# Kernel tuning notes

Measured on AMD Instinct MI355X. Metric: run time of the kernel, lower is better.

Reference implementation:

```python
import jax, jax.numpy as jnp
import numpy as np
import math

B, L, HID = 2, 2048, 1024
NH, DH = 16, 64
MASK_VAL = -1000000000.0  # half_precision_flag == False


def setup_inputs() -> dict:
    key = jax.random.key(0)
    ks = jax.random.split(key, 12)
    s = 0.02
    return {
        "queries": jax.random.normal(ks[0], (B, L, HID), jnp.float32),
        "keys": jax.random.normal(ks[1], (B, L, HID), jnp.float32),
        "values": jax.random.normal(ks[2], (B, L, HID), jnp.float32),
        "mask": jax.random.randint(ks[3], (B, L, L), 0, 2, jnp.int32),
        "Wq": jax.random.normal(ks[4], (HID, NH * DH), jnp.float32) * s,
        "bq": jnp.zeros((NH * DH,), jnp.float32),
        "Wk": jax.random.normal(ks[5], (HID, NH * DH), jnp.float32) * s,
        "bk": jnp.zeros((NH * DH,), jnp.float32),
        "Wv": jax.random.normal(ks[6], (HID, NH * DH), jnp.float32) * s,
        "bv": jnp.zeros((NH * DH,), jnp.float32),
        "Wo": jax.random.normal(ks[7], (NH * DH, HID), jnp.float32) * s,
        "bo": jnp.zeros((HID,), jnp.float32),
    }


def reference(queries, keys, values, mask, Wq, bq, Wk, bk, Wv, bv, Wo, bo):
    # Linear projections: (B, L, NH*DH)
    q = queries @ Wq + bq
    k = keys @ Wk + bk
    v = values @ Wv + bv
    # FAITHFUL to original: raw .view(B, NH, -1, DH) without transpose
    q = q.reshape(B, NH, L, DH)
    k = k.reshape(B, NH, L, DH)
    v = v.reshape(B, NH, L, DH)
    # scaled dot-product scores: (B, NH, L, L)
    scores = jnp.einsum("bhqd,bhkd->bhqk", q, k) / math.sqrt(DH)
    scores = jnp.where(mask[:, None, :, :] == 0, MASK_VAL, scores)
    probs = jax.nn.softmax(scores, axis=-1)  # dropout p=0 -> identity
    ctx = jnp.einsum("bhqk,bhkd->bhqd", probs, v)  # (B, NH, L, DH)
    # transpose(1,2) then flatten heads, as in original
    ctx = ctx.transpose(0, 2, 1, 3).reshape(B, L, NH * DH)
    return ctx @ Wo + bo
```

## Files before the change

kernel.cpp:

```cpp
#include <hip/hip_runtime.h>
#include <stdint.h>

typedef __bf16 bf16;
typedef __bf16 bf16x8 __attribute__((ext_vector_type(8)));
typedef __bf16 bf16x4 __attribute__((ext_vector_type(4)));
typedef float  f32x4  __attribute__((ext_vector_type(4)));
typedef short  s16x4  __attribute__((ext_vector_type(4)));
typedef unsigned long long ull;

#define GLOAD16(gptr, lptr)                                                     \
  __builtin_amdgcn_global_load_lds(                                             \
      (const __attribute__((address_space(1))) void*)(gptr),                    \
      (__attribute__((address_space(3))) void*)(lptr), 16, 0, 0)

#define MFMA16(a, b, c) __builtin_amdgcn_mfma_f32_16x16x32_bf16((a), (b), (c), 0, 0, 0)
#define MFMA16K16(a, b, c) __builtin_amdgcn_mfma_f32_16x16x16bf16_1k((a), (b), (c), 0, 0, 0)

static constexpr int B_ = 2, L_ = 2048, NH_ = 16, DH_ = 64;
static constexpr float QSCALE = 0.18033688011112042f;

__global__ void k_cvt3(const float* __restrict__ q, const float* __restrict__ k,
                       const float* __restrict__ v, bf16* __restrict__ outbase) {
  const float* in = blockIdx.y == 0 ? q : (blockIdx.y == 1 ? k : v);
  bf16* out = outbase + (size_t)blockIdx.y * 4194304;
  int i = blockIdx.x * blockDim.x + threadIdx.x;
  const float4 f = ((const float4*)in)[i];
  bf16x4 o = {(bf16)f.x, (bf16)f.y, (bf16)f.z, (bf16)f.w};
  ((bf16x4*)out)[i] = o;
}

__global__ void k_wtrans4(const float* __restrict__ wq, const float* __restrict__ wk,
                          const float* __restrict__ wv, const float* __restrict__ wo,
                          bf16* __restrict__ outbase) {
  const int z = blockIdx.z;
  const float* in = z == 0 ? wq : (z == 1 ? wk : (z == 2 ? wv : wo));
  bf16* out = outbase + (size_t)z * 1048576;
  __shared__ float t[32][33];
  int bx = blockIdx.x * 32, by = blockIdx.y * 32;
  int x = threadIdx.x & 31, y = threadIdx.x >> 5;
#pragma unroll
  for (int r = 0; r < 4; ++r)
    t[y + r * 8][x] = in[(size_t)(by + y + r * 8) * 1024 + bx + x];
  __syncthreads();
#pragma unroll
  for (int r = 0; r < 4; ++r)
    out[(size_t)(bx + y + r * 8) * 1024 + by + x] = (bf16)t[x][y + r * 8];
}

__global__ void k_maskbits(const int* __restrict__ mask, ull* __restrict__ mb) {
  int t = blockIdx.x * blockDim.x + threadIdx.x;
  ull bal = __ballot(mask[t] != 0);
  if ((threadIdx.x & 63) == 0) mb[t >> 6] = bal;
}

__global__ __launch_bounds__(256) void k_gemm3(const bf16* __restrict__ Xb,
                                               const bf16* __restrict__ Wb,
                                               const float* __restrict__ b0,
                                               const float* __restrict__ b1,
                                               const float* __restrict__ b2,
                                               bf16* __restrict__ Ob) {
  const int z = blockIdx.z;
  const bf16* A  = Xb + (size_t)z * 4194304;
  const bf16* Bt = Wb + (size_t)z * 1048576;
  const float* bias = z == 0 ? b0 : (z == 1 ? b1 : b2);
  bf16* C = Ob + (size_t)z * 4194304;
  const int m0 = blockIdx.y * 128, n0 = blockIdx.x * 128;
  __shared__ __align__(16) bf16 As[128 * 64];
  __shared__ __align__(16) bf16 Bs[128 * 64];
  const int tid = threadIdx.x, lane = tid & 63, w = tid >> 6, quad = lane >> 4, l15 = lane & 15;
  const int wm = (w & 1) * 64, wn = (w >> 1) * 64;
  f32x4 acc[4][4] = {};
  for (int kt = 0; kt < 16; ++kt) {
    const int kk = kt * 64;
#pragma unroll
    for (int i = 0; i < 4; ++i) {
      int s = tid + i * 256;
      int r = s >> 3, c = (s & 7) ^ (r & 7);
      GLOAD16(A + (size_t)(m0 + r) * 1024 + kk + c * 8, As + s * 8);
      GLOAD16(Bt + (size_t)(n0 + r) * 1024 + kk + c * 8, Bs + s * 8);
    }
    __syncthreads();
#pragma unroll
    for (int ks = 0; ks < 2; ++ks) {
      bf16x8 af[4], bb[4];
#pragma unroll
      for (int i = 0; i < 4; ++i) {
        int ra = wm + i * 16 + l15, rb = wn + i * 16 + l15;
        af[i] = *(const bf16x8*)(As + (ra * 8 + ((ks * 4 + quad) ^ (ra & 7))) * 8);
        bb[i] = *(const bf16x8*)(Bs + (rb * 8 + ((ks * 4 + quad) ^ (rb & 7))) * 8);
      }
#pragma unroll
      for (int mi = 0; mi < 4; ++mi)
#pragma unroll
        for (int ni = 0; ni < 4; ++ni)
          acc[mi][ni] = MFMA16(af[mi], bb[ni], acc[mi][ni]);
    }
    __syncthreads();
  }
  const float scale = (z == 0) ? QSCALE : 1.0f;
#pragma unroll
  for (int mi = 0; mi < 4; ++mi)
#pragma unroll
    for (int ni = 0; ni < 4; ++ni) {
      int row = m0 + wm + mi * 16 + quad * 4;
      int col = n0 + wn + ni * 16 + l15;
      float bz = bias[col];
      if (z == 2) {
        int b_ = row >> 11, l = row & 2047;
        int hh = l >> 7;
        int i0 = (l & 127) * 16 + (col >> 6);
        int d  = col & 63;
        bf16* dst = C + (size_t)(b_ * 16 + hh) * 131072;
#pragma unroll
        for (int r = 0; r < 4; ++r) {
          int iK = i0 + 16 * r;
          dst[((size_t)(iK >> 2) * 64 + d) * 4 + (iK & 3)] = (bf16)(acc[mi][ni][r] + bz);
        }
      } else {
#pragma unroll
        for (int r = 0; r < 4; ++r)
          C[(size_t)(row + r) * 1024 + col] = (bf16)((acc[mi][ni][r] + bz) * scale);
      }
    }
}

__global__ __launch_bounds__(256) void k_gemmo(const bf16* __restrict__ A,
                                               const bf16* __restrict__ Bt,
                                               const float* __restrict__ bias,
                                               float* __restrict__ C) {
  const int m0 = blockIdx.y * 64, n0 = blockIdx.x * 128;
  __shared__ __align__(16) bf16 As[64 * 32];
  __shared__ __align__(16) bf16 Bs[128 * 32];
  const int tid = threadIdx.x, lane = tid & 63, w = tid >> 6, quad = lane >> 4, l15 = lane & 15;
  const int wn = w * 32;
  f32x4 acc[4][2] = {};
  for (int kt = 0; kt < 32; ++kt) {
    const int kk = kt * 32;
    {
      int r = tid >> 2, c = (tid & 3) ^ ((r >> 1) & 3);
      GLOAD16(A + (size_t)(m0 + r) * 1024 + kk + c * 8, As + tid * 8);
    }
#pragma unroll
    for (int i = 0; i < 2; ++i) {
      int s = tid + i * 256;
      int r = s >> 2, c = (s & 3) ^ ((r >> 1) & 3);
      GLOAD16(Bt + (size_t)(n0 + r) * 1024 + kk + c * 8, Bs + s * 8);
    }
    __syncthreads();
    bf16x8 af[4], bb[2];
#pragma unroll
    for (int i = 0; i < 4; ++i) {
      int ra = i * 16 + l15;
      af[i] = *(const bf16x8*)(As + (ra * 4 + (quad ^ ((ra >> 1) & 3))) * 8);
    }
#pragma unroll
    for (int i = 0; i < 2; ++i) {
      int rb = wn + i * 16 + l15;
      bb[i] = *(const bf16x8*)(Bs + (rb * 4 + (quad ^ ((rb >> 1) & 3))) * 8);
    }
#pragma unroll
    for (int mi = 0; mi < 4; ++mi)
#pragma unroll
      for (int ni = 0; ni < 2; ++ni)
        acc[mi][ni] = MFMA16(af[mi], bb[ni], acc[mi][ni]);
    __syncthreads();
  }
#pragma unroll
  for (int mi = 0; mi < 4; ++mi)
#pragma unroll
    for (int ni = 0; ni < 2; ++ni) {
      int row = m0 + mi * 16 + quad * 4;
      int col = n0 + wn + ni * 16 + l15;
      float bz = bias[col];
#pragma unroll
      for (int r = 0; r < 4; ++r)
        C[(size_t)(row + r) * 1024 + col] = acc[mi][ni][r] + bz;
    }
}

__global__ __launch_bounds__(256) void k_flash(const bf16* __restrict__ Qp,
                                               const bf16* __restrict__ Kp,
                                               const bf16* __restrict__ Vtp,
                                               const ull* __restrict__ mb,
                                               bf16* __restrict__ ctx) {
  const int b = blockIdx.z, h = blockIdx.y, q0 = blockIdx.x * 64;
  const size_t HEAD = 131072;
  const bf16* Q  = Qp  + ((size_t)b * NH_ + h) * HEAD;
  const bf16* K  = Kp  + ((size_t)b * NH_ + h) * HEAD;
  const bf16* Vt = Vtp + ((size_t)b * NH_ + h) * HEAD;
  const ull* mrow = mb + (size_t)b * L_ * 32;

  __shared__ __align__(16) bf16 Ks[2][64 * 64];
  __shared__ __align__(16) bf16 Vs[2][64 * 64];
  __shared__ __align__(16) ull  Ms[2][128];

  const int tid = threadIdx.x, lane = tid & 63, w = tid >> 6, quad = lane >> 4, l15 = lane & 15;

  bf16x8 qf[2];
#pragma unroll
  for (int ks = 0; ks < 2; ++ks)
    qf[ks] = *(const bf16x8*)(Q + (size_t)(q0 + w * 16 + l15) * 64 + ks * 32 + quad * 8);

#pragma unroll
  for (int i = 0; i < 2; ++i) {
    int s = tid + i * 256;
    int key = s >> 3, c = (s & 7) ^ (key & 7);
    GLOAD16(K + (size_t)key * 64 + c * 8, Ks[0] + s * 8);
    GLOAD16(Vt + (size_t)s * 8, Vs[0] + s * 8);
  }
  if (w == 0) GLOAD16(mrow + (size_t)(q0 + lane) * 32, (bf16*)&Ms[0][0] + lane * 8);
  __syncthreads();

  f32x4 accO[4] = {};
  f32x4 accL = {};
  const s16x4 onesf = {0x3F80, 0x3F80, 0x3F80, 0x3F80};

  for (int kt = 0; kt < 32; ++kt) {
    const int cur = kt & 1;
    if (kt + 1 < 32) {
      const int nxt = cur ^ 1;
#pragma unroll
      for (int i = 0; i < 2; ++i) {
        int s = tid + i * 256;
        int key = s >> 3, c = (s & 7) ^ (key & 7);
        GLOAD16(K + (size_t)((kt + 1) * 64 + key) * 64 + c * 8, Ks[nxt] + s * 8);
        GLOAD16(Vt + (size_t)(kt + 1) * 4096 + s * 8, Vs[nxt] + s * 8);
      }
      if ((kt & 1) && w == 0)
        GLOAD16(mrow + (size_t)(q0 + lane) * 32 + (kt + 1),
                (bf16*)&Ms[((kt + 1) >> 1) & 1][0] + lane * 8);
    }

    f32x4 st[4] = {};
#pragma unroll
    for (int ks = 0; ks < 2; ++ks)
#pragma unroll
      for (int kb = 0; kb < 4; ++kb) {
        int key = kb * 16 + l15;
        bf16x8 kf = *(const bf16x8*)(Ks[cur] + (key * 8 + ((ks * 4 + quad) ^ (key & 7))) * 8);
        st[kb] = MFMA16(kf, qf[ks], st[kb]);
      }

    const ull word = Ms[(kt >> 1) & 1][(w * 16 + l15) * 2 + cur];
    s16x4 pf[4];
#pragma unroll
    for (int kb = 0; kb < 4; ++kb) {
      const unsigned nib = (unsigned)(word >> (kb * 16 + quad * 4)) & 0xFu;
      float p0 = (nib & 1u) ? __builtin_amdgcn_exp2f(st[kb][0]) : 0.f;
      float p1 = (nib & 2u) ? __builtin_amdgcn_exp2f(st[kb][1]) : 0.f;
      float p2 = (nib & 4u) ? __builtin_amdgcn_exp2f(st[kb][2]) : 0.f;
      float p3 = (nib & 8u) ? __builtin_amdgcn_exp2f(st[kb][3]) : 0.f;
      bf16x4 pb = {(bf16)p0, (bf16)p1, (bf16)p2, (bf16)p3};
      pf[kb] = __builtin_bit_cast(s16x4, pb);
    }

#pragma unroll
    for (int kb = 0; kb < 4; ++kb)
      accL = MFMA16K16(pf[kb], onesf, accL);

#pragma unroll
    for (int kb = 0; kb < 4; ++kb)
#pragma unroll
      for (int db = 0; db < 4; ++db) {
        s16x4 vf = *(const s16x4*)(Vs[cur] + ((size_t)((kb * 4 + quad) * 64 + db * 16 + l15)) * 4);
        accO[db] = MFMA16K16(pf[kb], vf, accO[db]);
      }
    __syncthreads();
  }

  float rl[4];
#pragma unroll
  for (int r = 0; r < 4; ++r) rl[r] = 1.0f / accL[r];
#pragma unroll
  for (int db = 0; db < 4; ++db) {
    const int col = h * 64 + db * 16 + l15;
#pragma unroll
    for (int r = 0; r < 4; ++r) {
      const int rowg = q0 + w * 16 + quad * 4 + r;
      ctx[((size_t)b * L_ + rowg) * 1024 + col] = (bf16)(accO[db][r] * rl[r]);
    }
  }
}

extern "C" void kernel_launch(void* const* d_in, const int* in_sizes, int n_in,
                              void* d_out, int out_size, void* d_ws, size_t ws_size,
                              hipStream_t stream) {
  (void)in_sizes; (void)n_in; (void)out_size; (void)ws_size;
  const float* q    = (const float*)d_in[0];
  const float* k    = (const float*)d_in[1];
  const float* v    = (const float*)d_in[2];
  const int*   mask = (const int*)d_in[3];
  const float* Wq = (const float*)d_in[4];
  const float* bq = (const float*)d_in[5];
  const float* Wk = (const float*)d_in[6];
  const float* bk = (const float*)d_in[7];
  const float* Wv = (const float*)d_in[8];
  const float* bv = (const float*)d_in[9];
  const float* Wo = (const float*)d_in[10];
  const float* bo = (const float*)d_in[11];
  float* out = (float*)d_out;

  char* ws = (char*)d_ws;
  const size_t SX = (size_t)4096 * 1024 * 2;
  const size_t SW = (size_t)1024 * 1024 * 2;
  bf16* X   = (bf16*)(ws);
  bf16* Wt  = (bf16*)(ws + 3 * SX);
  bf16* QKV = (bf16*)(ws + 3 * SX + 4 * SW);
  bf16* Qp  = QKV;
  bf16* Kp  = QKV + 4194304;
  bf16* Vtp = QKV + 2 * 4194304;
  bf16* Ctx = (bf16*)(ws + 6 * SX + 4 * SW);
  ull* mbits = (ull*)(ws + 7 * SX + 4 * SW);

  dim3 blk(256);
  k_cvt3<<<dim3(4096, 3), blk, 0, stream>>>(q, k, v, X);
  k_wtrans4<<<dim3(32, 32, 4), blk, 0, stream>>>(Wq, Wk, Wv, Wo, Wt);
  k_maskbits<<<32768, blk, 0, stream>>>(mask, mbits);

  k_gemm3<<<dim3(8, 32, 3), blk, 0, stream>>>(X, Wt, bq, bk, bv, QKV);

  k_flash<<<dim3(32, NH_, B_), blk, 0, stream>>>(Qp, Kp, Vtp, mbits, Ctx);

  k_gemmo<<<dim3(8, 64), blk, 0, stream>>>(Ctx, Wt + 3 * 1048576, bo, out);
}
```

Baseline: 291.0 us.

## Merge prep kernels, halve QKV GEMM K-tile, read flash K/V directly from global

```diff
diff --git a/kernel.cpp b/kernel.cpp
--- a/kernel.cpp
+++ b/kernel.cpp
@@ -19,38 +19,47 @@
 static constexpr int B_ = 2, L_ = 2048, NH_ = 16, DH_ = 64;
 static constexpr float QSCALE = 0.18033688011112042f;
 
-__global__ void k_cvt3(const float* __restrict__ q, const float* __restrict__ k,
-                       const float* __restrict__ v, bf16* __restrict__ outbase) {
-  const float* in = blockIdx.y == 0 ? q : (blockIdx.y == 1 ? k : v);
-  bf16* out = outbase + (size_t)blockIdx.y * 4194304;
-  int i = blockIdx.x * blockDim.x + threadIdx.x;
-  const float4 f = ((const float4*)in)[i];
-  bf16x4 o = {(bf16)f.x, (bf16)f.y, (bf16)f.z, (bf16)f.w};
-  ((bf16x4*)out)[i] = o;
-}
-
-__global__ void k_wtrans4(const float* __restrict__ wq, const float* __restrict__ wk,
-                          const float* __restrict__ wv, const float* __restrict__ wo,
-                          bf16* __restrict__ outbase) {
-  const int z = blockIdx.z;
-  const float* in = z == 0 ? wq : (z == 1 ? wk : (z == 2 ? wv : wo));
-  bf16* out = outbase + (size_t)z * 1048576;
+__global__ __launch_bounds__(256) void k_prep(const float* __restrict__ q,
+                                              const float* __restrict__ k,
+                                              const float* __restrict__ v,
+                                              const int* __restrict__ mask,
+                                              const float* __restrict__ wq,
+                                              const float* __restrict__ wk,
+                                              const float* __restrict__ wv,
+                                              const float* __restrict__ wo,
+                                              bf16* __restrict__ X,
+                                              bf16* __restrict__ Wt,
+                                              ull* __restrict__ mb) {
   __shared__ float t[32][33];
-  int bx = blockIdx.x * 32, by = blockIdx.y * 32;
-  int x = threadIdx.x & 31, y = threadIdx.x >> 5;
-#pragma unroll
-  for (int r = 0; r < 4; ++r)
-    t[y + r * 8][x] = in[(size_t)(by + y + r * 8) * 1024 + bx + x];
-  __syncthreads();
-#pragma unroll
-  for (int r = 0; r < 4; ++r)
-    out[(size_t)(bx + y + r * 8) * 1024 + by + x] = (bf16)t[x][y + r * 8];
-}
-
-__global__ void k_maskbits(const int* __restrict__ mask, ull* __restrict__ mb) {
-  int t = blockIdx.x * blockDim.x + threadIdx.x;
-  ull bal = __ballot(mask[t] != 0);
-  if ((threadIdx.x & 63) == 0) mb[t >> 6] = bal;
+  const int bid = blockIdx.x, tid = threadIdx.x;
+  if (bid < 32768) {
+    int tt = bid * 256 + tid;
+    ull bal = __ballot(mask[tt] != 0);
+    if ((tid & 63) == 0) mb[tt >> 6] = bal;
+  } else if (bid < 45056) {
+    int u = bid - 32768;
+    int z = u >> 12, x = u & 4095;
+    const float* in = z == 0 ? q : (z == 1 ? k : v);
+    bf16* out = X + (size_t)z * 4194304;
+    int i = x * 256 + tid;
+    const float4 f = ((const float4*)in)[i];
+    bf16x4 o = {(bf16)f.x, (bf16)f.y, (bf16)f.z, (bf16)f.w};
+    ((bf16x4*)out)[i] = o;
+  } else {
+    int u = bid - 45056;
+    int z = u >> 10, rem = u & 1023;
+    const float* in = z == 0 ? wq : (z == 1 ? wk : (z == 2 ? wv : wo));
+    bf16* out = Wt + (size_t)z * 1048576;
+    int bx = (rem & 31) * 32, by = (rem >> 5) * 32;
+    int x = tid & 31, y = tid >> 5;
+#pragma unroll
+    for (int r = 0; r < 4; ++r)
+      t[y + r * 8][x] = in[(size_t)(by + y + r * 8) * 1024 + bx + x];
+    __syncthreads();
+#pragma unroll
+    for (int r = 0; r < 4; ++r)
+      out[(size_t)(bx + y + r * 8) * 1024 + by + x] = (bf16)t[x][y + r * 8];
+  }
 }
 
 __global__ __launch_bounds__(256) void k_gemm3(const bf16* __restrict__ Xb,
@@ -65,36 +74,33 @@
   const float* bias = z == 0 ? b0 : (z == 1 ? b1 : b2);
   bf16* C = Ob + (size_t)z * 4194304;
   const int m0 = blockIdx.y * 128, n0 = blockIdx.x * 128;
-  __shared__ __align__(16) bf16 As[128 * 64];
-  __shared__ __align__(16) bf16 Bs[128 * 64];
+  __shared__ __align__(16) bf16 As[128 * 32];
+  __shared__ __align__(16) bf16 Bs[128 * 32];
   const int tid = threadIdx.x, lane = tid & 63, w = tid >> 6, quad = lane >> 4, l15 = lane & 15;
   const int wm = (w & 1) * 64, wn = (w >> 1) * 64;
   f32x4 acc[4][4] = {};
-  for (int kt = 0; kt < 16; ++kt) {
-    const int kk = kt * 64;
-#pragma unroll
-    for (int i = 0; i < 4; ++i) {
+  for (int kt = 0; kt < 32; ++kt) {
+    const int kk = kt * 32;
+#pragma unroll
+    for (int i = 0; i < 2; ++i) {
       int s = tid + i * 256;
-      int r = s >> 3, c = (s & 7) ^ (r & 7);
+      int r = s >> 2, c = (s & 3) ^ ((r >> 1) & 3);
       GLOAD16(A + (size_t)(m0 + r) * 1024 + kk + c * 8, As + s * 8);
       GLOAD16(Bt + (size_t)(n0 + r) * 1024 + kk + c * 8, Bs + s * 8);
     }
     __syncthreads();
-#pragma unroll
-    for (int ks = 0; ks < 2; ++ks) {
-      bf16x8 af[4], bb[4];
-#pragma unroll
-      for (int i = 0; i < 4; ++i) {
-        int ra = wm + i * 16 + l15, rb = wn + i * 16 + l15;
-        af[i] = *(const bf16x8*)(As + (ra * 8 + ((ks * 4 + quad) ^ (ra & 7))) * 8);
-        bb[i] = *(const bf16x8*)(Bs + (rb * 8 + ((ks * 4 + quad) ^ (rb & 7))) * 8);
-      }
-#pragma unroll
-      for (int mi = 0; mi < 4; ++mi)
-#pragma unroll
-        for (int ni = 0; ni < 4; ++ni)
-          acc[mi][ni] = MFMA16(af[mi], bb[ni], acc[mi][ni]);
-    }
+    bf16x8 af[4], bb[4];
+#pragma unroll
+    for (int i = 0; i < 4; ++i) {
+      int ra = wm + i * 16 + l15, rb = wn + i * 16 + l15;
+      af[i] = *(const bf16x8*)(As + (ra * 4 + (quad ^ ((ra >> 1) & 3))) * 8);
+      bb[i] = *(const bf16x8*)(Bs + (rb * 4 + (quad ^ ((rb >> 1) & 3))) * 8);
+    }
+#pragma unroll
+    for (int mi = 0; mi < 4; ++mi)
+#pragma unroll
+      for (int ni = 0; ni < 4; ++ni)
+        acc[mi][ni] = MFMA16(af[mi], bb[ni], acc[mi][ni]);
     __syncthreads();
   }
   const float scale = (z == 0) ? QSCALE : 1.0f;
@@ -188,11 +194,6 @@
   const bf16* Q  = Qp  + ((size_t)b * NH_ + h) * HEAD;
   const bf16* K  = Kp  + ((size_t)b * NH_ + h) * HEAD;
   const bf16* Vt = Vtp + ((size_t)b * NH_ + h) * HEAD;
-  const ull* mrow = mb + (size_t)b * L_ * 32;
-
-  __shared__ __align__(16) bf16 Ks[2][64 * 64];
-  __shared__ __align__(16) bf16 Vs[2][64 * 64];
-  __shared__ __align__(16) ull  Ms[2][128];
 
   const int tid = threadIdx.x, lane = tid & 63, w = tid >> 6, quad = lane >> 4, l15 = lane & 15;
 
@@ -201,47 +202,23 @@
   for (int ks = 0; ks < 2; ++ks)
     qf[ks] = *(const bf16x8*)(Q + (size_t)(q0 + w * 16 + l15) * 64 + ks * 32 + quad * 8);
 
-#pragma unroll
-  for (int i = 0; i < 2; ++i) {
-    int s = tid + i * 256;
-    int key = s >> 3, c = (s & 7) ^ (key & 7);
-    GLOAD16(K + (size_t)key * 64 + c * 8, Ks[0] + s * 8);
-    GLOAD16(Vt + (size_t)s * 8, Vs[0] + s * 8);
-  }
-  if (w == 0) GLOAD16(mrow + (size_t)(q0 + lane) * 32, (bf16*)&Ms[0][0] + lane * 8);
-  __syncthreads();
+  const ull* mlane = mb + (size_t)b * L_ * 32 + (size_t)(q0 + w * 16 + l15) * 32;
 
   f32x4 accO[4] = {};
   f32x4 accL = {};
   const s16x4 onesf = {0x3F80, 0x3F80, 0x3F80, 0x3F80};
 
   for (int kt = 0; kt < 32; ++kt) {
-    const int cur = kt & 1;
-    if (kt + 1 < 32) {
-      const int nxt = cur ^ 1;
-#pragma unroll
-      for (int i = 0; i < 2; ++i) {
-        int s = tid + i * 256;
-        int key = s >> 3, c = (s & 7) ^ (key & 7);
-        GLOAD16(K + (size_t)((kt + 1) * 64 + key) * 64 + c * 8, Ks[nxt] + s * 8);
-        GLOAD16(Vt + (size_t)(kt + 1) * 4096 + s * 8, Vs[nxt] + s * 8);
-      }
-      if ((kt & 1) && w == 0)
-        GLOAD16(mrow + (size_t)(q0 + lane) * 32 + (kt + 1),
-                (bf16*)&Ms[((kt + 1) >> 1) & 1][0] + lane * 8);
-    }
-
     f32x4 st[4] = {};
 #pragma unroll
     for (int ks = 0; ks < 2; ++ks)
 #pragma unroll
       for (int kb = 0; kb < 4; ++kb) {
-        int key = kb * 16 + l15;
-        bf16x8 kf = *(const bf16x8*)(Ks[cur] + (key * 8 + ((ks * 4 + quad) ^ (key & 7))) * 8);
+        bf16x8 kf = *(const bf16x8*)(K + (size_t)(kt * 64 + kb * 16 + l15) * 64 + ks * 32 + quad * 8);
         st[kb] = MFMA16(kf, qf[ks], st[kb]);
       }
 
-    const ull word = Ms[(kt >> 1) & 1][(w * 16 + l15) * 2 + cur];
+    const ull word = mlane[kt];
     s16x4 pf[4];
 #pragma unroll
     for (int kb = 0; kb < 4; ++kb) {
@@ -262,10 +239,10 @@
     for (int kb = 0; kb < 4; ++kb)
 #pragma unroll
       for (int db = 0; db < 4; ++db) {
-        s16x4 vf = *(const s16x4*)(Vs[cur] + ((size_t)((kb * 4 + quad) * 64 + db * 16 + l15)) * 4);
+        s16x4 vf = *(const s16x4*)(Vt + (size_t)kt * 4096 +
+                                   ((size_t)((kb * 4 + quad) * 64 + db * 16 + l15)) * 4);
         accO[db] = MFMA16K16(pf[kb], vf, accO[db]);
       }
-    __syncthreads();
   }
 
   float rl[4];
@@ -313,9 +290,7 @@
   ull* mbits = (ull*)(ws + 7 * SX + 4 * SW);
 
   dim3 blk(256);
-  k_cvt3<<<dim3(4096, 3), blk, 0, stream>>>(q, k, v, X);
-  k_wtrans4<<<dim3(32, 32, 4), blk, 0, stream>>>(Wq, Wk, Wv, Wo, Wt);
-  k_maskbits<<<32768, blk, 0, stream>>>(mask, mbits);
+  k_prep<<<49152, blk, 0, stream>>>(q, k, v, mask, Wq, Wk, Wv, Wo, X, Wt, mbits);
 
   k_gemm3<<<dim3(8, 32, 3), blk, 0, stream>>>(X, Wt, bq, bk, bv, QKV);
 
```

New measurement: 395.6 us. +35.9%, slower.
